# Performance work log

Hardware: AMD Instinct MI355X
Metric: run time of the kernel (lower is better)

Reference implementation:

```python
import jax, jax.numpy as jnp
import numpy as np

B, S, E, H, L = 4, 8192, 1024, 16, 64
D = E // H

def setup_inputs() -> dict:
    key = jax.random.key(0)
    ks = jax.random.split(key, 8)
    scale = 1.0 / np.sqrt(E)
    inp = {
        'query': jax.random.normal(ks[0], (B, S, E), jnp.float32),
        'key':   jax.random.normal(ks[1], (B, S, E), jnp.float32),
        'value': jax.random.normal(ks[2], (B, S, E), jnp.float32),
        'Wq': jax.random.normal(ks[3], (E, E), jnp.float32) * scale,
        'bq': jnp.zeros((E,), jnp.float32),
        'Wk': jax.random.normal(ks[4], (E, E), jnp.float32) * scale,
        'bk': jnp.zeros((E,), jnp.float32),
        'Wv': jax.random.normal(ks[5], (E, E), jnp.float32) * scale,
        'bv': jnp.zeros((E,), jnp.float32),
        'Wo': jax.random.normal(ks[6], (E, E), jnp.float32) * scale,
        'bo': jnp.zeros((E,), jnp.float32),
    }
    return inp

def reference(query, key, value, Wq, bq, Wk, bk, Wv, bv, Wo, bo):
    b, s, _ = query.shape
    # projections (torch Linear: x @ W.T + b), split heads -> [B, H, S, D]
    def split(x):
        return x.reshape(b, s, H, D).transpose(0, 2, 1, 3)
    q = split(query @ Wq.T + bq)
    k = split(key   @ Wk.T + bk)
    v = split(value @ Wv.T + bv)
    # landmark selection: key-norms averaged over heads -> [B, S], topk L per batch
    scores = jnp.linalg.norm(k, axis=-1).mean(axis=1)        # [B, S]
    _, idx = jax.lax.top_k(scores, L)                        # [B, L]
    # gather landmark K/V -> [B, H, L, D]
    gidx = idx[:, None, :, None]                             # [B, 1, L, 1]
    k_sp = jnp.take_along_axis(k, gidx, axis=2)
    v_sp = jnp.take_along_axis(v, gidx, axis=2)
    # attention over landmarks only
    attn = jnp.einsum('bhsd,bhld->bhsl', q, k_sp) / jnp.sqrt(jnp.asarray(D, q.dtype))
    w = jax.nn.softmax(attn, axis=-1)                        # [B, H, S, L]
    out = jnp.einsum('bhsl,bhld->bhsd', w, v_sp)             # [B, H, S, D]
    out = out.transpose(0, 2, 1, 3).reshape(b, s, E)
    out = out @ Wo.T + bo
    return (out, w)
```

## Files before the change

kernel.cpp:

```cpp
#include <hip/hip_runtime.h>
#include <cstdint>

typedef unsigned short u16;
typedef __attribute__((ext_vector_type(8))) short short8;
typedef __attribute__((ext_vector_type(4))) float f32x4;

#define AS1 __attribute__((address_space(1)))
#define AS3 __attribute__((address_space(3)))

#define BB 4
#define SS 8192
#define EE 1024
#define HH 16
#define DD 64
#define LL 64
#define CANDN 96

__device__ __forceinline__ void async16(const void* g, void* l) {
  __builtin_amdgcn_global_load_lds((const AS1 uint32_t*)g, (AS3 uint32_t*)l, 16, 0, 0);
}
__device__ __forceinline__ u16 f2b(float f) {
  uint32_t u = __float_as_uint(f);
  return (u16)((u + 0x7fffu + ((u >> 16) & 1u)) >> 16);
}
__device__ __forceinline__ float b2f(u16 h) { return __uint_as_float(((uint32_t)h) << 16); }

__global__ __launch_bounds__(256) void cvt_bf16_k(const float* __restrict__ in, u16* __restrict__ out, int n4) {
  int i = blockIdx.x * 256 + threadIdx.x;
  if (i >= n4) return;
  float4 v = ((const float4*)in)[i];
  ushort4 o;
  o.x = f2b(v.x); o.y = f2b(v.y); o.z = f2b(v.z); o.w = f2b(v.w);
  ((ushort4*)out)[i] = o;
}

#define FENCE_RW()  asm volatile("s_waitcnt lgkmcnt(0)\n\ts_barrier" ::: "memory")
#define FENCE_V6()  asm volatile("s_waitcnt vmcnt(6)\n\ts_barrier" ::: "memory")
#define FENCE_V0()  asm volatile("s_waitcnt vmcnt(0)\n\ts_barrier" ::: "memory")

__global__ __launch_bounds__(512) void gemm256(const u16* __restrict__ A, const u16* __restrict__ W,
                                               const float* __restrict__ bias,
                                               float* __restrict__ Cf, u16* __restrict__ Cb, int K) {
  extern __shared__ __align__(16) u16 lds_[];
  u16* lA = lds_;
  u16* lB = lds_ + 32768;
  const int tid = threadIdx.x;
  const int wv = tid >> 6, lane = tid & 63;
  const int quad = lane >> 4, l15 = lane & 15;
  const int wm = wv >> 1, wn = wv & 1;

  const int nwg = gridDim.x * gridDim.y;
  int g = blockIdx.y * gridDim.x + blockIdx.x;
  int bx = blockIdx.x, by = blockIdx.y;
  if ((nwg & 7) == 0) {
    const int chunk = nwg >> 3;
    const int v = (g & 7) * chunk + (g >> 3);
    bx = v % gridDim.x;
    by = v / gridDim.x;
  }
  const int mt = by * 256, nt = bx * 128;

  const int rl = tid >> 3;
  const int g8 = (((tid & 7) ^ (rl & 7))) * 8;
  const u16* sA00 = A + (size_t)(mt + rl) * K + g8;
  const u16* sA01 = A + (size_t)(mt + 64 + rl) * K + g8;
  const u16* sA10 = A + (size_t)(mt + 128 + rl) * K + g8;
  const u16* sA11 = A + (size_t)(mt + 192 + rl) * K + g8;
  const u16* sB0  = W + (size_t)(nt + rl) * K + g8;
  const u16* sB1  = W + (size_t)(nt + 64 + rl) * K + g8;
  const int dA = tid * 8;
  const int dB = tid * 8;

  auto STAGE = [&](int tile, int pb) {
    const int off = tile * 64;
    async16(sA00 + off, lA + pb * 16384 + dA);
    async16(sA01 + off, lA + pb * 16384 + dA + 4096);
    async16(sA10 + off, lA + pb * 16384 + 8192 + dA);
    async16(sA11 + off, lA + pb * 16384 + 8192 + dA + 4096);
    async16(sB0 + off, lB + pb * 8192 + dB);
    async16(sB1 + off, lB + pb * 8192 + dB + 4096);
  };

  f32x4 acc[4][4];
#pragma unroll
  for (int i = 0; i < 4; i++)
#pragma unroll
    for (int j = 0; j < 4; j++) acc[i][j] = (f32x4){0.f, 0.f, 0.f, 0.f};

  const int NT = K >> 6;
  STAGE(0, 0);
  STAGE(1, 1);
  FENCE_V6();

  for (int t = 0; t < NT; ++t) {
    const int pb = t & 1;
    const short8* pA = (const short8*)(lA + pb * 16384);
    const short8* pB = (const short8*)(lB + pb * 8192);
    short8 af[2][4], bf[2][4];
#pragma unroll
    for (int i = 0; i < 4; i++) {
      const int r = 64 * wm + 16 * i + l15;
      af[0][i] = pA[r * 8 + (quad ^ (r & 7))];
      af[1][i] = pA[r * 8 + ((quad + 4) ^ (r & 7))];
      const int rb = 64 * wn + 16 * i + l15;
      bf[0][i] = pB[rb * 8 + (quad ^ (rb & 7))];
      bf[1][i] = pB[rb * 8 + ((quad + 4) ^ (rb & 7))];
    }
#pragma unroll
    for (int i = 0; i < 4; i++)
#pragma unroll
      for (int j = 0; j < 4; j++)
        acc[i][j] = __builtin_amdgcn_mfma_f32_16x16x32_bf16(af[0][i], bf[0][j], acc[i][j], 0, 0, 0);
    FENCE_RW();
    if (t + 2 < NT) STAGE(t + 2, pb);
#pragma unroll
    for (int i = 0; i < 4; i++)
#pragma unroll
      for (int j = 0; j < 4; j++)
        acc[i][j] = __builtin_amdgcn_mfma_f32_16x16x32_bf16(af[1][i], bf[1][j], acc[i][j], 0, 0, 0);
    if (t + 1 < NT) {
      if (t + 1 == NT - 1) { FENCE_V0(); } else { FENCE_V6(); }
    }
  }

#pragma unroll
  for (int j = 0; j < 4; j++) {
    int gn = nt + 64 * wn + 16 * j + l15;
    float bs = bias[gn];
#pragma unroll
    for (int i = 0; i < 4; i++) {
#pragma unroll
      for (int r = 0; r < 4; r++) {
        int gm = mt + 64 * wm + 16 * i + quad * 4 + r;
        float v = acc[i][j][r] + bs;
        if (Cf) Cf[(size_t)gm * EE + gn] = v;
        if (Cb) Cb[(size_t)gm * EE + gn] = f2b(v);
      }
    }
  }
}

__global__ __launch_bounds__(256) void scores_k(const u16* __restrict__ kb, float* __restrict__ sc) {
  const int row = blockIdx.x;
  const int wv = threadIdx.x >> 6, lane = threadIdx.x & 63;
  __shared__ float part[4];
  float acc = 0.f;
  const u16* base = kb + (size_t)row * EE;
#pragma unroll
  for (int hh = 0; hh < 4; hh++) {
    float v = b2f(base[(wv * 4 + hh) * 64 + lane]);
    float s = v * v;
#pragma unroll
    for (int m = 1; m < 64; m <<= 1) s += __shfl_xor(s, m, 64);
    acc += sqrtf(s);
  }
  if (lane == 0) part[wv] = acc;
  __syncthreads();
  if (threadIdx.x == 0) sc[row] = (part[0] + part[1] + part[2] + part[3]) * (1.f / 16.f);
}

#define TKT 1024
#define EQCAP 256
__global__ __launch_bounds__(TKT) void topk1_k(const float* __restrict__ sc, int* __restrict__ cand) {
  const int b = blockIdx.x;
  __shared__ uint32_t s[SS];
  __shared__ int wsum[TKT / 64];
  __shared__ int cnt_sh;
  __shared__ int counter, eqcount;
  __shared__ int eqbuf[EQCAP];
  const int tid = threadIdx.x;
  const int lane = tid & 63, wv = tid >> 6;
  for (int i = tid; i < SS; i += TKT) s[i] = __float_as_uint(sc[b * SS + i]);
  if (tid == 0) { counter = 0; eqcount = 0; }
  __syncthreads();

  uint32_t lo = 0u, hi = 0x7f7fffffu;
  while (lo < hi) {
    uint32_t mid = lo + ((hi - lo + 1) >> 1);
    int c = 0;
    for (int i = tid; i < SS; i += TKT) c += (s[i] >= mid) ? 1 : 0;
#pragma unroll
    for (int m = 1; m < 64; m <<= 1) c += __shfl_xor(c, m, 64);
    if (lane == 0) wsum[wv] = c;
    __syncthreads();
    if (tid == 0) {
      int t = 0;
#pragma unroll
      for (int w = 0; w < TKT / 64; w++) t += wsum[w];
      cnt_sh = t;
    }
    __syncthreads();
    if (cnt_sh >= CANDN) lo = mid; else hi = mid - 1;
    __syncthreads();
  }
  const uint32_t T = lo;

  for (int i = tid; i < SS; i += TKT) {
    uint32_t u = s[i];
    if (u > T) {
      int p = atomicAdd(&counter, 1);
      cand[b * CANDN + p] = i;
    } else if (u == T) {
      int p = atomicAdd(&eqcount, 1);
      if (p < EQCAP) eqbuf[p] = i;
    }
  }
  __syncthreads();
  const int above = counter;
  const int rem = CANDN - above;
  int ec = eqcount; if (ec > EQCAP) ec = EQCAP;
  __syncthreads();
  for (int i = tid; i < ec; i += TKT) {
    int me = eqbuf[i];
    int rank = 0;
    for (int j = 0; j < ec; j++) rank += (eqbuf[j] < me) ? 1 : 0;
    if (rank < rem) {
      int p = atomicAdd(&counter, 1);
      cand[b * CANDN + p] = me;
    }
  }
}

__global__ __launch_bounds__(256) void rescore_k(const float* __restrict__ key, const float* __restrict__ Wk,
                                                 const int* __restrict__ cand, double* __restrict__ kpart) {
  const int kc = blockIdx.x, h = blockIdx.y, b = blockIdx.z;
  const int d = threadIdx.x & 63, cg = threadIdx.x >> 6;
  __shared__ float wk[64 * 257];
  __shared__ float xs[24 * 256];
  for (int i = threadIdx.x; i < 64 * 256; i += 256)
    wk[(i >> 8) * 257 + (i & 255)] = Wk[(size_t)(h * 64 + (i >> 8)) * EE + kc * 256 + (i & 255)];
  for (int c0 = 0; c0 < CANDN; c0 += 24) {
    __syncthreads();
    for (int i = threadIdx.x; i < 24 * 256; i += 256) {
      int c = c0 + (i >> 8);
      xs[i] = key[((size_t)b * SS + cand[b * CANDN + c]) * EE + kc * 256 + (i & 255)];
    }
    __syncthreads();
    double acc[6] = {0, 0, 0, 0, 0, 0};
    for (int kk = 0; kk < 256; kk++) {
      double wv_ = (double)wk[d * 257 + kk];
#pragma unroll
      for (int j = 0; j < 6; j++)
        acc[j] += wv_ * (double)xs[(cg * 6 + j) * 256 + kk];
    }
#pragma unroll
    for (int j = 0; j < 6; j++) {
      int c = c0 + cg * 6 + j;
      kpart[(((size_t)kc * BB + b) * CANDN + c) * 1024 + h * 64 + d] = acc[j];
    }
  }
}

__global__ __launch_bounds__(64) void score2_k(const double* __restrict__ kpart, const float* __restrict__ bk,
                                               double* __restrict__ sc2) {
  const int c = blockIdx.x, b = blockIdx.y;
  const int lane = threadIdx.x;
  double tot = 0.0;
  for (int h = 0; h < HH; h++) {
    double v = (double)bk[h * 64 + lane];
#pragma unroll
    for (int kc = 0; kc < 4; kc++)
      v += kpart[(((size_t)kc * BB + b) * CANDN + c) * 1024 + h * 64 + lane];
    double s = v * v;
#pragma unroll
    for (int m = 1; m < 64; m <<= 1) s += __shfl_xor(s, m, 64);
    tot += sqrt(s);
  }
  if (lane == 0) sc2[b * CANDN + c] = tot * (1.0 / 16.0);
}

__global__ __launch_bounds__(128) void topk2_k(const double* __restrict__ sc2, const int* __restrict__ cand,
                                               int* __restrict__ idxf) {
  const int b = blockIdx.x, t = threadIdx.x;
  if (t >= CANDN) return;
  double my = sc2[b * CANDN + t];
  int mi = cand[b * CANDN + t];
  int rank = 0;
  for (int j = 0; j < CANDN; j++) {
    double sj = sc2[b * CANDN + j];
    int ij = cand[b * CANDN + j];
    if (sj > my || (sj == my && ij < mi)) rank++;
  }
  if (rank < LL) idxf[b * LL + rank] = mi;
}

__global__ __launch_bounds__(256) void gatherx_k(const float* __restrict__ value, const int* __restrict__ idxf,
                                                 u16* __restrict__ xg) {
  const int r = blockIdx.x;
  const int b = r >> 6;
  const float* src = value + ((size_t)b * SS + idxf[r]) * EE;
  for (int i = threadIdx.x; i < EE; i += 256) xg[(size_t)r * EE + i] = f2b(src[i]);
}

__global__ __launch_bounds__(64) void gathersp_k(const u16* __restrict__ kb, const float* __restrict__ vg,
                                                 const int* __restrict__ idxf,
                                                 u16* __restrict__ ksp, u16* __restrict__ vspT) {
  const int g = blockIdx.x;
  const int l = g & 63, h = (g >> 6) & 15, b = g >> 10;
  const int d = threadIdx.x;
  ksp[(size_t)g * 64 + d] = kb[((size_t)b * SS + idxf[b * 64 + l]) * EE + h * 64 + d];
  vspT[((size_t)(b * 16 + h) * 64 + d) * 64 + l] = f2b(vg[((size_t)b * 64 + l) * EE + h * 64 + d]);
}

__global__ __launch_bounds__(256) void attn_k(const u16* __restrict__ qb, const u16* __restrict__ ksp,
                                              const u16* __restrict__ vspT,
                                              float* __restrict__ wout, u16* __restrict__ attnb) {
  __shared__ __align__(16) u16 qt[4096];
  __shared__ __align__(16) u16 kt[4096];
  __shared__ __align__(16) u16 vt[4096];
  __shared__ __align__(16) u16 wt[4096];
  const int tid = threadIdx.x;
  const int wv = tid >> 6, lane = tid & 63, quad = lane >> 4, l15 = lane & 15;
  const int s0 = blockIdx.x * 64;
  const int bh = blockIdx.y, b = bh >> 4, h = bh & 15;

  {
    const int bi0 = tid, bi1 = 256 + tid;
    const int r0 = bi0 >> 3, c0 = (bi0 & 7) ^ (r0 & 7);
    const int r1 = bi1 >> 3, c1 = (bi1 & 7) ^ (r1 & 7);
    const u16* qg = qb + ((size_t)b * SS + s0) * EE + h * 64;
    async16(qg + (size_t)r0 * EE + c0 * 8, qt + bi0 * 8);
    async16(qg + (size_t)r1 * EE + c1 * 8, qt + bi1 * 8);
    const u16* kg = ksp + (size_t)bh * 4096;
    async16(kg + r0 * 64 + c0 * 8, kt + bi0 * 8);
    async16(kg + r1 * 64 + c1 * 8, kt + bi1 * 8);
    const u16* vgp = vspT + (size_t)bh * 4096;
    async16(vgp + r0 * 64 + c0 * 8, vt + bi0 * 8);
    async16(vgp + r1 * 64 + c1 * 8, vt + bi1 * 8);
  }
  __syncthreads();

  f32x4 acc[4];
#pragma unroll
  for (int j = 0; j < 4; j++) acc[j] = (f32x4){0.f, 0.f, 0.f, 0.f};
  const int ar = 16 * wv + l15;
#pragma unroll
  for (int ks = 0; ks < 2; ks++) {
    const int cg = quad + ks * 4;
    short8 af = ((const short8*)qt)[ar * 8 + (cg ^ (ar & 7))];
#pragma unroll
    for (int j = 0; j < 4; j++) {
      int br = 16 * j + l15;
      short8 bf = ((const short8*)kt)[br * 8 + (cg ^ (br & 7))];
      acc[j] = __builtin_amdgcn_mfma_f32_16x16x32_bf16(af, bf, acc[j], 0, 0, 0);
    }
  }
#pragma unroll
  for (int j = 0; j < 4; j++) acc[j] *= 0.125f;

  float inv[4];
#pragma unroll
  for (int r = 0; r < 4; r++) {
    float m = fmaxf(fmaxf(acc[0][r], acc[1][r]), fmaxf(acc[2][r], acc[3][r]));
#pragma unroll
    for (int msk = 1; msk < 16; msk <<= 1) m = fmaxf(m, __shfl_xor(m, msk, 64));
    float e0 = __expf(acc[0][r] - m);
    float e1 = __expf(acc[1][r] - m);
    float e2 = __expf(acc[2][r] - m);
    float e3 = __expf(acc[3][r] - m);
    acc[0][r] = e0; acc[1][r] = e1; acc[2][r] = e2; acc[3][r] = e3;
    float s = e0 + e1 + e2 + e3;
#pragma unroll
    for (int msk = 1; msk < 16; msk <<= 1) s += __shfl_xor(s, msk, 64);
    inv[r] = 1.f / s;
  }

  const size_t wbase = ((size_t)bh * SS + s0 + 16 * wv) * 64;
#pragma unroll
  for (int j = 0; j < 4; j++) {
#pragma unroll
    for (int r = 0; r < 4; r++) {
      float val = acc[j][r] * inv[r];
      int rowl = quad * 4 + r;
      int l = 16 * j + l15;
      wout[wbase + (size_t)rowl * 64 + l] = val;
      int wr = 16 * wv + rowl;
      wt[wr * 64 + ((l >> 3) ^ (wr & 7)) * 8 + (l & 7)] = f2b(val);
    }
  }
  __syncthreads();

  f32x4 acc2[4];
#pragma unroll
  for (int j = 0; j < 4; j++) acc2[j] = (f32x4){0.f, 0.f, 0.f, 0.f};
#pragma unroll
  for (int ks = 0; ks < 2; ks++) {
    const int cg = quad + ks * 4;
    short8 af = ((const short8*)wt)[ar * 8 + (cg ^ (ar & 7))];
#pragma unroll
    for (int j = 0; j < 4; j++) {
      int br = 16 * j + l15;
      short8 bf = ((const short8*)vt)[br * 8 + (cg ^ (br & 7))];
      acc2[j] = __builtin_amdgcn_mfma_f32_16x16x32_bf16(af, bf, acc2[j], 0, 0, 0);
    }
  }
#pragma unroll
  for (int j = 0; j < 4; j++)
#pragma unroll
    for (int r = 0; r < 4; r++)
      attnb[((size_t)b * SS + s0 + 16 * wv + quad * 4 + r) * EE + h * 64 + 16 * j + l15] = f2b(acc2[j][r]);
}

extern "C" void kernel_launch(void* const* d_in, const int* in_sizes, int n_in,
                              void* d_out, int out_size, void* d_ws, size_t ws_size,
                              hipStream_t stream) {
  (void)in_sizes; (void)n_in; (void)out_size; (void)ws_size;
  const float* query = (const float*)d_in[0];
  const float* key   = (const float*)d_in[1];
  const float* value = (const float*)d_in[2];
  const float* Wq = (const float*)d_in[3];
  const float* bq = (const float*)d_in[4];
  const float* Wk = (const float*)d_in[5];
  const float* bk = (const float*)d_in[6];
  const float* Wv = (const float*)d_in[7];
  const float* bv = (const float*)d_in[8];
  const float* Wo = (const float*)d_in[9];
  const float* bo = (const float*)d_in[10];
  float* out = (float*)d_out;
  float* wout = out + (size_t)BB * SS * EE;

  char* p = (char*)d_ws;
  auto alloc = [&](size_t n) { char* r = p; p += (n + 255) & ~(size_t)255; return r; };
  u16* qbf = (u16*)alloc((size_t)BB * SS * EE * 2);
  u16* kbf = (u16*)alloc((size_t)BB * SS * EE * 2);
  u16* wqb = (u16*)alloc((size_t)EE * EE * 2);
  u16* wkb = (u16*)alloc((size_t)EE * EE * 2);
  u16* wvb = (u16*)alloc((size_t)EE * EE * 2);
  u16* wob = (u16*)alloc((size_t)EE * EE * 2);
  u16* qb  = (u16*)alloc((size_t)BB * SS * EE * 2);
  u16* kb  = (u16*)alloc((size_t)BB * SS * EE * 2);
  float*  sc    = (float*)alloc((size_t)BB * SS * 4);
  int*    cand  = (int*)alloc(BB * CANDN * 4);
  double* kpart = (double*)alloc((size_t)4 * BB * CANDN * 1024 * 8);
  double* sc2   = (double*)alloc(BB * CANDN * 8);
  int*    idxf  = (int*)alloc(BB * LL * 4);
  u16*    xg    = (u16*)alloc((size_t)BB * LL * EE * 2);
  float*  vg    = (float*)alloc((size_t)BB * LL * EE * 4);
  u16*    ksp   = (u16*)alloc((size_t)BB * HH * LL * DD * 2);
  u16*    vspT  = (u16*)alloc((size_t)BB * HH * DD * LL * 2);
  u16*    attnb = qbf;

  const int M = BB * SS;
  const size_t gemm_lds = 98304;

  cvt_bf16_k<<<(M * EE / 4 + 255) / 256, 256, 0, stream>>>(query, qbf, M * EE / 4);
  cvt_bf16_k<<<(M * EE / 4 + 255) / 256, 256, 0, stream>>>(key, kbf, M * EE / 4);
  cvt_bf16_k<<<(EE * EE / 4 + 255) / 256, 256, 0, stream>>>(Wq, wqb, EE * EE / 4);
  cvt_bf16_k<<<(EE * EE / 4 + 255) / 256, 256, 0, stream>>>(Wk, wkb, EE * EE / 4);
  cvt_bf16_k<<<(EE * EE / 4 + 255) / 256, 256, 0, stream>>>(Wv, wvb, EE * EE / 4);
  cvt_bf16_k<<<(EE * EE / 4 + 255) / 256, 256, 0, stream>>>(Wo, wob, EE * EE / 4);

  dim3 gg(EE / 128, M / 256);
  gemm256<<<gg, 512, gemm_lds, stream>>>(qbf, wqb, bq, nullptr, qb, EE);
  gemm256<<<gg, 512, gemm_lds, stream>>>(kbf, wkb, bk, nullptr, kb, EE);

  scores_k<<<M, 256, 0, stream>>>(kb, sc);
  topk1_k<<<BB, TKT, 0, stream>>>(sc, cand);
  rescore_k<<<dim3(4, HH, BB), 256, 0, stream>>>(key, Wk, cand, kpart);
  score2_k<<<dim3(CANDN, BB), 64, 0, stream>>>(kpart, bk, sc2);
  topk2_k<<<BB, 128, 0, stream>>>(sc2, cand, idxf);

  gatherx_k<<<BB * LL, 256, 0, stream>>>(value, idxf, xg);
  gemm256<<<dim3(EE / 128, BB * LL / 256), 512, gemm_lds, stream>>>(xg, wvb, bv, vg, nullptr, EE);
  gathersp_k<<<BB * HH * LL, 64, 0, stream>>>(kb, vg, idxf, ksp, vspT);

  attn_k<<<dim3(SS / 64, BB * HH), 256, 0, stream>>>(qb, ksp, vspT, wout, attnb);

  gemm256<<<gg, 512, gemm_lds, stream>>>(attnb, wob, bo, out, nullptr, EE);
}
```

Before: 1.006 ms.

## Fuse fp32-to-bf16 conversion and key-norm scoring into Q/K projection GEMMs

Adds a GEMM variant that reads the fp32 query/key activations directly, converting them to bf16 in registers before writing them to LDS. This removes the two separate full-size conversion kernels and their intermediate bf16 buffers. The K projection epilogue also computes per-head L2 norms via shuffles and atomically accumulates the head-averaged score, which replaces the separate scores kernel and needs a memset of the score buffer. In exchange, A-tile loads go through registers instead of async global-to-LDS copies and read twice the bytes per tile, and the score sums now depend on atomic ordering, which may perturb top-k near ties.

```diff
diff --git a/kernel.cpp b/kernel.cpp
--- a/kernel.cpp
+++ b/kernel.cpp
@@ -140,23 +140,132 @@
   }
 }
 
-__global__ __launch_bounds__(256) void scores_k(const u16* __restrict__ kb, float* __restrict__ sc) {
-  const int row = blockIdx.x;
-  const int wv = threadIdx.x >> 6, lane = threadIdx.x & 63;
-  __shared__ float part[4];
-  float acc = 0.f;
-  const u16* base = kb + (size_t)row * EE;
-#pragma unroll
-  for (int hh = 0; hh < 4; hh++) {
-    float v = b2f(base[(wv * 4 + hh) * 64 + lane]);
-    float s = v * v;
-#pragma unroll
-    for (int m = 1; m < 64; m <<= 1) s += __shfl_xor(s, m, 64);
-    acc += sqrtf(s);
-  }
-  if (lane == 0) part[wv] = acc;
-  __syncthreads();
-  if (threadIdx.x == 0) sc[row] = (part[0] + part[1] + part[2] + part[3]) * (1.f / 16.f);
+__global__ __launch_bounds__(512) void gemm_qk(const float* __restrict__ A, const u16* __restrict__ W,
+                                               const float* __restrict__ bias,
+                                               u16* __restrict__ Cb, float* __restrict__ scA, int K) {
+  extern __shared__ __align__(16) u16 lds_[];
+  u16* lA = lds_;
+  u16* lB = lds_ + 32768;
+  const int tid = threadIdx.x;
+  const int wv = tid >> 6, lane = tid & 63;
+  const int quad = lane >> 4, l15 = lane & 15;
+  const int wm = wv >> 1, wn = wv & 1;
+
+  const int nwg = gridDim.x * gridDim.y;
+  int g = blockIdx.y * gridDim.x + blockIdx.x;
+  int bx = blockIdx.x, by = blockIdx.y;
+  if ((nwg & 7) == 0) {
+    const int chunk = nwg >> 3;
+    const int v = (g & 7) * chunk + (g >> 3);
+    bx = v % gridDim.x;
+    by = v / gridDim.x;
+  }
+  const int mt = by * 256, nt = bx * 128;
+
+  const int rl = tid >> 3, g7 = tid & 7;
+  const int K4 = K >> 2;
+  const float4* pA4 = (const float4*)A + (size_t)(mt + rl) * K4 + 2 * g7;
+  const int g8 = (g7 ^ (rl & 7)) * 8;
+  const u16* sB0 = W + (size_t)(nt + rl) * K + g8;
+  const u16* sB1 = W + (size_t)(nt + 64 + rl) * K + g8;
+  const int dB = tid * 8;
+
+  float4 ra[4][2];
+  auto LOADA = [&](int t) {
+#pragma unroll
+    for (int rr = 0; rr < 4; rr++) {
+      const float4* p = pA4 + (size_t)rr * 64 * K4 + t * 16;
+      ra[rr][0] = p[0];
+      ra[rr][1] = p[1];
+    }
+  };
+  auto STAGEB = [&](int t, int pb) {
+    async16(sB0 + t * 64, lB + pb * 8192 + dB);
+    async16(sB1 + t * 64, lB + pb * 8192 + dB + 4096);
+  };
+  auto CONVW = [&](int pb) {
+    u16* dst = lA + pb * 16384;
+#pragma unroll
+    for (int rr = 0; rr < 4; rr++) {
+      uint32_t u0, u1, u2, u3;
+      asm("v_cvt_pk_bf16_f32 %0, %1, %2" : "=v"(u0) : "v"(ra[rr][0].x), "v"(ra[rr][0].y));
+      asm("v_cvt_pk_bf16_f32 %0, %1, %2" : "=v"(u1) : "v"(ra[rr][0].z), "v"(ra[rr][0].w));
+      asm("v_cvt_pk_bf16_f32 %0, %1, %2" : "=v"(u2) : "v"(ra[rr][1].x), "v"(ra[rr][1].y));
+      asm("v_cvt_pk_bf16_f32 %0, %1, %2" : "=v"(u3) : "v"(ra[rr][1].z), "v"(ra[rr][1].w));
+      const int row = rl + 64 * rr;
+      const int xg = g7 ^ (row & 7);
+      int4 pk; pk.x = (int)u0; pk.y = (int)u1; pk.z = (int)u2; pk.w = (int)u3;
+      *(int4*)(dst + row * 64 + xg * 8) = pk;
+    }
+  };
+
+  f32x4 acc[4][4];
+#pragma unroll
+  for (int i = 0; i < 4; i++)
+#pragma unroll
+    for (int j = 0; j < 4; j++) acc[i][j] = (f32x4){0.f, 0.f, 0.f, 0.f};
+
+  const int NT = K >> 6;
+  LOADA(0); STAGEB(0, 0);
+  CONVW(0);
+  LOADA(1); STAGEB(1, 1);
+  asm volatile("s_waitcnt lgkmcnt(0) vmcnt(10)\n\ts_barrier" ::: "memory");
+
+  for (int t = 0; t < NT; ++t) {
+    const int pb = t & 1;
+    const short8* qA = (const short8*)(lA + pb * 16384);
+    const short8* qB = (const short8*)(lB + pb * 8192);
+    short8 af[2][4], bf[2][4];
+#pragma unroll
+    for (int i = 0; i < 4; i++) {
+      const int r = 64 * wm + 16 * i + l15;
+      af[0][i] = qA[r * 8 + (quad ^ (r & 7))];
+      af[1][i] = qA[r * 8 + ((quad + 4) ^ (r & 7))];
+      const int rb = 64 * wn + 16 * i + l15;
+      bf[0][i] = qB[rb * 8 + (quad ^ (rb & 7))];
+      bf[1][i] = qB[rb * 8 + ((quad + 4) ^ (rb & 7))];
+    }
+#pragma unroll
+    for (int i = 0; i < 4; i++)
+#pragma unroll
+      for (int j = 0; j < 4; j++)
+        acc[i][j] = __builtin_amdgcn_mfma_f32_16x16x32_bf16(af[0][i], bf[0][j], acc[i][j], 0, 0, 0);
+    FENCE_RW();
+    if (t + 1 < NT) CONVW(pb ^ 1);
+    if (t + 2 < NT) { LOADA(t + 2); STAGEB(t + 2, pb); }
+#pragma unroll
+    for (int i = 0; i < 4; i++)
+#pragma unroll
+      for (int j = 0; j < 4; j++)
+        acc[i][j] = __builtin_amdgcn_mfma_f32_16x16x32_bf16(af[1][i], bf[1][j], acc[i][j], 0, 0, 0);
+    if (t + 1 < NT) {
+      if (t + 2 < NT) { asm volatile("s_waitcnt lgkmcnt(0) vmcnt(10)\n\ts_barrier" ::: "memory"); }
+      else            { asm volatile("s_waitcnt lgkmcnt(0) vmcnt(0)\n\ts_barrier" ::: "memory"); }
+    }
+  }
+
+  float bs[4];
+#pragma unroll
+  for (int j = 0; j < 4; j++) bs[j] = bias[nt + 64 * wn + 16 * j + l15];
+#pragma unroll
+  for (int i = 0; i < 4; i++) {
+#pragma unroll
+    for (int r = 0; r < 4; r++) {
+      const int gm = mt + 64 * wm + 16 * i + quad * 4 + r;
+      float nrm = 0.f;
+#pragma unroll
+      for (int j = 0; j < 4; j++) {
+        float v = acc[i][j][r] + bs[j];
+        Cb[(size_t)gm * EE + (nt + 64 * wn + 16 * j + l15)] = f2b(v);
+        nrm += v * v;
+      }
+      if (scA) {
+#pragma unroll
+        for (int m = 1; m < 16; m <<= 1) nrm += __shfl_xor(nrm, m, 64);
+        if (l15 == 0) atomicAdd(&scA[gm], sqrtf(nrm) * (1.f / 16.f));
+      }
+    }
+  }
 }
 
 #define TKT 1024
@@ -443,18 +552,16 @@
   const int M = BB * SS;
   const size_t gemm_lds = 98304;
 
-  cvt_bf16_k<<<(M * EE / 4 + 255) / 256, 256, 0, stream>>>(query, qbf, M * EE / 4);
-  cvt_bf16_k<<<(M * EE / 4 + 255) / 256, 256, 0, stream>>>(key, kbf, M * EE / 4);
   cvt_bf16_k<<<(EE * EE / 4 + 255) / 256, 256, 0, stream>>>(Wq, wqb, EE * EE / 4);
   cvt_bf16_k<<<(EE * EE / 4 + 255) / 256, 256, 0, stream>>>(Wk, wkb, EE * EE / 4);
   cvt_bf16_k<<<(EE * EE / 4 + 255) / 256, 256, 0, stream>>>(Wv, wvb, EE * EE / 4);
   cvt_bf16_k<<<(EE * EE / 4 + 255) / 256, 256, 0, stream>>>(Wo, wob, EE * EE / 4);
+  hipMemsetAsync(sc, 0, (size_t)M * 4, stream);
 
   dim3 gg(EE / 128, M / 256);
-  gemm256<<<gg, 512, gemm_lds, stream>>>(qbf, wqb, bq, nullptr, qb, EE);
-  gemm256<<<gg, 512, gemm_lds, stream>>>(kbf, wkb, bk, nullptr, kb, EE);
-
-  scores_k<<<M, 256, 0, stream>>>(kb, sc);
+  gemm_qk<<<gg, 512, gemm_lds, stream>>>(query, wqb, bq, qb, nullptr, EE);
+  gemm_qk<<<gg, 512, gemm_lds, stream>>>(key, wkb, bk, kb, sc, EE);
+
   topk1_k<<<BB, TKT, 0, stream>>>(sc, cand);
   rescore_k<<<dim3(4, HH, BB), 256, 0, stream>>>(key, Wk, cand, kpart);
   score2_k<<<dim3(CANDN, BB), 64, 0, stream>>>(kpart, bk, sc2);
```

Measured after the change: 993.7 us. No clear change (-1.2%).

## Fuse fp32-to-bf16 input conversion and key-norm scoring into Q/K projection GEMMs

Applied to the files above, without the earlier changes.

Adds a new GEMM kernel that reads fp32 query/key activations directly, converts them to bf16 in registers with packed convert instructions, and stages them into swizzled LDS. Weights still arrive through async global-to-LDS loads, and a software pipeline overlaps loads with MFMA work. The K projection epilogue also computes per-head L2 norms and atomically accumulates the head-averaged score. This removes the two large bf16 conversion passes, their intermediate buffers, and the separate scores kernel. The cost is twice the global read bytes for A inside the GEMM, atomics with a memset, and a smaller 128x128 tile than the previous 256-row GEMM.

```diff
diff --git a/kernel.cpp b/kernel.cpp
--- a/kernel.cpp
+++ b/kernel.cpp
@@ -140,23 +140,125 @@
   }
 }
 
-__global__ __launch_bounds__(256) void scores_k(const u16* __restrict__ kb, float* __restrict__ sc) {
-  const int row = blockIdx.x;
-  const int wv = threadIdx.x >> 6, lane = threadIdx.x & 63;
-  __shared__ float part[4];
-  float acc = 0.f;
-  const u16* base = kb + (size_t)row * EE;
-#pragma unroll
-  for (int hh = 0; hh < 4; hh++) {
-    float v = b2f(base[(wv * 4 + hh) * 64 + lane]);
-    float s = v * v;
-#pragma unroll
-    for (int m = 1; m < 64; m <<= 1) s += __shfl_xor(s, m, 64);
-    acc += sqrtf(s);
-  }
-  if (lane == 0) part[wv] = acc;
-  __syncthreads();
-  if (threadIdx.x == 0) sc[row] = (part[0] + part[1] + part[2] + part[3]) * (1.f / 16.f);
+#define LOADA(T, P) { const float4* _p = pA4 + (size_t)(T) * 8; \
+  ra[P][0] = _p[0]; ra[P][1] = _p[1]; ra[P][2] = _p[2]; ra[P][3] = _p[3]; }
+#define CVTA(P) { \
+  asm("v_cvt_pk_bf16_f32 %0, %1, %2" : "=v"(pk0.x) : "v"(ra[P][0].x), "v"(ra[P][0].y)); \
+  asm("v_cvt_pk_bf16_f32 %0, %1, %2" : "=v"(pk0.y) : "v"(ra[P][0].z), "v"(ra[P][0].w)); \
+  asm("v_cvt_pk_bf16_f32 %0, %1, %2" : "=v"(pk0.z) : "v"(ra[P][1].x), "v"(ra[P][1].y)); \
+  asm("v_cvt_pk_bf16_f32 %0, %1, %2" : "=v"(pk0.w) : "v"(ra[P][1].z), "v"(ra[P][1].w)); \
+  asm("v_cvt_pk_bf16_f32 %0, %1, %2" : "=v"(pk1.x) : "v"(ra[P][2].x), "v"(ra[P][2].y)); \
+  asm("v_cvt_pk_bf16_f32 %0, %1, %2" : "=v"(pk1.y) : "v"(ra[P][2].z), "v"(ra[P][2].w)); \
+  asm("v_cvt_pk_bf16_f32 %0, %1, %2" : "=v"(pk1.z) : "v"(ra[P][3].x), "v"(ra[P][3].y)); \
+  asm("v_cvt_pk_bf16_f32 %0, %1, %2" : "=v"(pk1.w) : "v"(ra[P][3].z), "v"(ra[P][3].w)); }
+#define QKBODY(T, P, Q) { \
+  const short8* pAl = (const short8*)lA[P]; \
+  const short8* pBl = (const short8*)lB[P]; \
+  short8 af[4], bfr[4]; \
+  _Pragma("unroll") for (int i = 0; i < 4; i++) { \
+    const int r = 64 * wm + 16 * i + l15; \
+    af[i] = pAl[r * 4 + (quad ^ ((r >> 1) & 3))]; \
+    const int rb = 64 * wn + 16 * i + l15; \
+    bfr[i] = pBl[rb * 4 + (quad ^ ((rb >> 1) & 3))]; \
+  } \
+  _Pragma("unroll") for (int i = 0; i < 4; i++) \
+    _Pragma("unroll") for (int j = 0; j < 4; j++) \
+      acc[i][j] = __builtin_amdgcn_mfma_f32_16x16x32_bf16(af[i], bfr[j], acc[i][j], 0, 0, 0); \
+  FENCE_RW(); \
+  if ((T) + 2 < NT) { \
+    *(int4*)(wdst0 + (P) * 4096) = pk0; \
+    *(int4*)(wdst1 + (P) * 4096) = pk1; \
+    async16(sB0 + ((T) + 2) * 32, &lB[P][tid * 8]); \
+    async16(sB1 + ((T) + 2) * 32, &lB[P][2048 + tid * 8]); \
+  } \
+  if ((T) + 4 < NT) LOADA((T) + 4, P) \
+  if ((T) + 3 < NT) CVTA(Q) \
+  if ((T) + 1 < NT) { if ((T) + 3 < NT) { FENCE_V6(); } else { FENCE_V0(); } } }
+
+__global__ __launch_bounds__(256, 5) void gemm_qk(const float* __restrict__ A, const u16* __restrict__ W,
+                                                  const float* __restrict__ bias,
+                                                  u16* __restrict__ Cb, float* __restrict__ scA, int K) {
+  __shared__ __align__(16) u16 lA[2][4096];
+  __shared__ __align__(16) u16 lB[2][4096];
+  const int tid = threadIdx.x;
+  const int wv = tid >> 6, lane = tid & 63;
+  const int quad = lane >> 4, l15 = lane & 15;
+  const int wm = wv >> 1, wn = wv & 1;
+
+  const int nwg = gridDim.x * gridDim.y;
+  int g = blockIdx.y * gridDim.x + blockIdx.x;
+  int bx = blockIdx.x, by = blockIdx.y;
+  if ((nwg & 7) == 0) {
+    const int chunk = nwg >> 3;
+    const int v = (g & 7) * chunk + (g >> 3);
+    bx = v % gridDim.x;
+    by = v / gridDim.x;
+  }
+  const int mt = by * 128, nt = bx * 128;
+
+  const int K4 = K >> 2;
+  const int ar_row = tid >> 1, ar_h = tid & 1;
+  const int asw = (ar_row >> 1) & 3;
+  const float4* pA4 = (const float4*)A + (size_t)(mt + ar_row) * K4 + 4 * ar_h;
+  u16* wdst0 = &lA[0][ar_row * 32 + ((2 * ar_h + 0) ^ asw) * 8];
+  u16* wdst1 = &lA[0][ar_row * 32 + ((2 * ar_h + 1) ^ asw) * 8];
+
+  const int brow0 = tid >> 2;
+  const int bg = (tid & 3) ^ ((brow0 >> 1) & 3);
+  const u16* sB0 = W + (size_t)(nt + brow0) * K + bg * 8;
+  const u16* sB1 = W + (size_t)(nt + 64 + brow0) * K + bg * 8;
+
+  float4 ra[2][4];
+  int4 pk0, pk1;
+
+  f32x4 acc[4][4];
+#pragma unroll
+  for (int i = 0; i < 4; i++)
+#pragma unroll
+    for (int j = 0; j < 4; j++) acc[i][j] = (f32x4){0.f, 0.f, 0.f, 0.f};
+
+  const int NT = K >> 5;
+
+  LOADA(0, 0) LOADA(1, 1)
+  async16(sB0, &lB[0][tid * 8]);
+  async16(sB1, &lB[0][2048 + tid * 8]);
+  async16(sB0 + 32, &lB[1][tid * 8]);
+  async16(sB1 + 32, &lB[1][2048 + tid * 8]);
+  CVTA(0)
+  *(int4*)wdst0 = pk0; *(int4*)wdst1 = pk1;
+  CVTA(1)
+  *(int4*)(wdst0 + 4096) = pk0; *(int4*)(wdst1 + 4096) = pk1;
+  LOADA(2, 0) LOADA(3, 1)
+  CVTA(0)
+  asm volatile("s_waitcnt lgkmcnt(0) vmcnt(8)\n\ts_barrier" ::: "memory");
+
+  for (int tt = 0; tt < NT; tt += 2) {
+    QKBODY(tt, 0, 1)
+    QKBODY(tt + 1, 1, 0)
+  }
+
+  float bs[4];
+#pragma unroll
+  for (int j = 0; j < 4; j++) bs[j] = bias[nt + 64 * wn + 16 * j + l15];
+#pragma unroll
+  for (int i = 0; i < 4; i++) {
+#pragma unroll
+    for (int r = 0; r < 4; r++) {
+      const int gm = mt + 64 * wm + 16 * i + quad * 4 + r;
+      float nrm = 0.f;
+#pragma unroll
+      for (int j = 0; j < 4; j++) {
+        float v = acc[i][j][r] + bs[j];
+        Cb[(size_t)gm * EE + (nt + 64 * wn + 16 * j + l15)] = f2b(v);
+        nrm += v * v;
+      }
+      if (scA) {
+#pragma unroll
+        for (int m = 1; m < 16; m <<= 1) nrm += __shfl_xor(nrm, m, 64);
+        if (l15 == 0) atomicAdd(&scA[gm], sqrtf(nrm) * (1.f / 16.f));
+      }
+    }
+  }
 }
 
 #define TKT 1024
@@ -443,18 +545,16 @@
   const int M = BB * SS;
   const size_t gemm_lds = 98304;
 
-  cvt_bf16_k<<<(M * EE / 4 + 255) / 256, 256, 0, stream>>>(query, qbf, M * EE / 4);
-  cvt_bf16_k<<<(M * EE / 4 + 255) / 256, 256, 0, stream>>>(key, kbf, M * EE / 4);
   cvt_bf16_k<<<(EE * EE / 4 + 255) / 256, 256, 0, stream>>>(Wq, wqb, EE * EE / 4);
   cvt_bf16_k<<<(EE * EE / 4 + 255) / 256, 256, 0, stream>>>(Wk, wkb, EE * EE / 4);
   cvt_bf16_k<<<(EE * EE / 4 + 255) / 256, 256, 0, stream>>>(Wv, wvb, EE * EE / 4);
   cvt_bf16_k<<<(EE * EE / 4 + 255) / 256, 256, 0, stream>>>(Wo, wob, EE * EE / 4);
-
-  dim3 gg(EE / 128, M / 256);
-  gemm256<<<gg, 512, gemm_lds, stream>>>(qbf, wqb, bq, nullptr, qb, EE);
-  gemm256<<<gg, 512, gemm_lds, stream>>>(kbf, wkb, bk, nullptr, kb, EE);
-
-  scores_k<<<M, 256, 0, stream>>>(kb, sc);
+  hipMemsetAsync(sc, 0, (size_t)M * 4, stream);
+
+  dim3 gq(EE / 128, M / 128);
+  gemm_qk<<<gq, 256, 0, stream>>>(query, wqb, bq, qb, nullptr, EE);
+  gemm_qk<<<gq, 256, 0, stream>>>(key, wkb, bk, kb, sc, EE);
+
   topk1_k<<<BB, TKT, 0, stream>>>(sc, cand);
   rescore_k<<<dim3(4, HH, BB), 256, 0, stream>>>(key, Wk, cand, kpart);
   score2_k<<<dim3(CANDN, BB), 64, 0, stream>>>(kpart, bk, sc2);
@@ -466,5 +566,5 @@
 
   attn_k<<<dim3(SS / 64, BB * HH), 256, 0, stream>>>(qb, ksp, vspT, wout, attnb);
 
-  gemm256<<<gg, 512, gemm_lds, stream>>>(attnb, wob, bo, out, nullptr, EE);
-}
+  gemm256<<<dim3(EE / 128, M / 256), 512, gemm_lds, stream>>>(attnb, wob, bo, out, nullptr, EE);
+}
```

Measured after the change: 2.345 ms. 133% more time.
